# Performance work log

Measured on AMD Instinct MI355X. Metric: run time of the kernel, lower is better.

## Reference

```python
import jax, jax.numpy as jnp
import numpy as np

N_NODES = 100000


def setup_inputs() -> dict:
    key = jax.random.key(0)
    ks = jax.random.split(key, 8)
    E = 1600000
    x = jax.random.normal(ks[0], (N_NODES, 128), dtype=jnp.float32)
    src = jax.random.randint(ks[1], (E,), 0, N_NODES, dtype=jnp.int32)
    dst = jax.random.randint(ks[2], (E,), 0, N_NODES, dtype=jnp.int32)
    s = 1.0 / np.sqrt(128.0)
    w_self = jax.random.normal(ks[3], (5, 128, 128), dtype=jnp.float32) * s
    w_neigh = jax.random.normal(ks[4], (5, 128, 128), dtype=jnp.float32) * s
    b = jnp.zeros((5, 128), dtype=jnp.float32)
    w_self_out = jax.random.normal(ks[5], (128, 47), dtype=jnp.float32) * s
    w_neigh_out = jax.random.normal(ks[6], (128, 47), dtype=jnp.float32) * s
    b_out = jnp.zeros((47,), dtype=jnp.float32)
    return {"x": x, "src": src, "dst": dst, "w_self": w_self, "w_neigh": w_neigh,
            "b": b, "w_self_out": w_self_out, "w_neigh_out": w_neigh_out, "b_out": b_out}


def _mean_agg(h, src, dst, inv_deg):
    # segment-sum of source features into destination nodes, then mean
    summed = jax.ops.segment_sum(h[src], dst, num_segments=N_NODES)  # [N, d]
    return summed * inv_deg[:, None]


def _sage_layer(h, src, dst, inv_deg, ws, wn, bias):
    neigh = _mean_agg(h, src, dst, inv_deg)
    return h @ ws + neigh @ wn + bias


def reference(x, src, dst, w_self, w_neigh, b, w_self_out, w_neigh_out, b_out):
    # in-degree, clamped to 1 for isolated nodes (DGL mean aggregator behavior)
    deg = jax.ops.segment_sum(jnp.ones_like(dst, dtype=x.dtype), dst, num_segments=N_NODES)
    inv_deg = 1.0 / jnp.maximum(deg, 1.0)

    # layer 0: no ReLU after (matches original forward)
    h = _sage_layer(x, src, dst, inv_deg, w_self[0], w_neigh[0], b[0])
    # layers 1..4: SAGEConv + ReLU
    for i in range(1, 5):
        h = _sage_layer(h, src, dst, inv_deg, w_self[i], w_neigh[i], b[i])
        h = jax.nn.relu(h)
    # final layer: 128 -> num_classes, no activation
    h = _sage_layer(h, src, dst, inv_deg, w_self_out, w_neigh_out, b_out)
    return h
```

## Files before the change

kernel.cpp:

```cpp
#include <hip/hip_runtime.h>

typedef float f4 __attribute__((ext_vector_type(4)));
typedef float f32x4 __attribute__((ext_vector_type(4)));
typedef float f2 __attribute__((ext_vector_type(2)));
typedef short s16x8 __attribute__((ext_vector_type(8)));
typedef int i4 __attribute__((ext_vector_type(4)));

#define N_NODES 100000
#define NBUCK 196
#define NB1 256

__device__ inline unsigned short f2bf(float f) {
    unsigned int u = __builtin_bit_cast(unsigned int, f);
    u += 0x7FFFu + ((u >> 16) & 1u);
    return (unsigned short)(u >> 16);
}
__device__ inline float bflo(unsigned int v) { return __builtin_bit_cast(float, v << 16); }
__device__ inline float bfhi(unsigned int v) { return __builtin_bit_cast(float, v & 0xFFFF0000u); }


__global__ __launch_bounds__(256) void k_hist(const int* __restrict__ dst,
                                              int* __restrict__ histG, int E) {
    __shared__ int h[NBUCK];
    int tid = threadIdx.x;
    for (int i = tid; i < NBUCK; i += 256) h[i] = 0;
    __syncthreads();
    int chunk = (E + NB1 - 1) / NB1;
    int s = blockIdx.x * chunk, eN = min(E, s + chunk);
    for (int i = s + tid; i < eN; i += 256) atomicAdd(&h[dst[i] >> 9], 1);
    __syncthreads();
    for (int i = tid; i < NBUCK; i += 256) histG[i * NB1 + blockIdx.x] = h[i];
}

__global__ __launch_bounds__(1024) void k_scanB(int* __restrict__ histG) {
    __shared__ int ps[1024];
    int t = threadIdx.x;
    int base = t * 49;
    int vals[49];
    int sum = 0;
#pragma unroll
    for (int i = 0; i < 49; ++i) { vals[i] = histG[base + i]; sum += vals[i]; }
    ps[t] = sum;
    __syncthreads();
    for (int off = 1; off < 1024; off <<= 1) {
        int v = (t >= off) ? ps[t - off] : 0;
        __syncthreads();
        ps[t] += v;
        __syncthreads();
    }
    int run = ps[t] - sum;
#pragma unroll
    for (int i = 0; i < 49; ++i) { int v = vals[i]; histG[base + i] = run; run += v; }
}

__global__ __launch_bounds__(256) void k_place(const int* __restrict__ src,
                                               const int* __restrict__ dst,
                                               const int* __restrict__ histG,
                                               unsigned int* __restrict__ ebuf, int E) {
    __shared__ int cur[NBUCK];
    int tid = threadIdx.x;
    for (int i = tid; i < NBUCK; i += 256) cur[i] = histG[i * NB1 + blockIdx.x];
    __syncthreads();
    int chunk = (E + NB1 - 1) / NB1;
    int s = blockIdx.x * chunk, eN = min(E, s + chunk);
    for (int i = s + tid; i < eN; i += 256) {
        int d = dst[i];
        int b = d >> 9;
        int pos = atomicAdd(&cur[b], 1);
        ebuf[pos] = (unsigned int)src[i] | ((unsigned int)(d & 511) << 17);
    }
}

__global__ __launch_bounds__(256) void k_csr(const unsigned int* __restrict__ ebuf,
                                             const int* __restrict__ histG,
                                             int* __restrict__ rp, int* __restrict__ col,
                                             float* __restrict__ invd, int N, int E) {
    __shared__ int ldeg[512];
    __shared__ int lbase[512];
    int b = blockIdx.x, tid = threadIdx.x;
    int base = histG[b * NB1];
    int endB = (b == NBUCK - 1) ? E : histG[(b + 1) * NB1];
    int cnt = endB - base;
    int n0 = b << 9;

    ldeg[tid] = 0;
    ldeg[tid + 256] = 0;
    __syncthreads();
    for (int i = tid; i < cnt; i += 256) atomicAdd(&ldeg[ebuf[base + i] >> 17], 1);
    __syncthreads();

    int a0 = ldeg[tid], a1 = ldeg[tid + 256];
    lbase[tid] = a0;
    lbase[tid + 256] = a1;
    __syncthreads();
    for (int off = 1; off < 512; off <<= 1) {
        int v0 = (tid >= off) ? lbase[tid - off] : 0;
        int v1 = (tid + 256 >= off) ? lbase[tid + 256 - off] : 0;
        __syncthreads();
        lbase[tid] += v0;
        lbase[tid + 256] += v1;
        __syncthreads();
    }
    int e0 = lbase[tid] - a0, e1 = lbase[tid + 256] - a1;
    __syncthreads();
    lbase[tid] = e0;
    lbase[tid + 256] = e1;
    ldeg[tid] = 0;
    ldeg[tid + 256] = 0;
    __syncthreads();

    for (int i = tid; i < cnt; i += 256) {
        unsigned int p = ebuf[base + i];
        int dl = p >> 17;
        int pos = base + lbase[dl] + atomicAdd(&ldeg[dl], 1);
        col[pos] = (int)(p & 0x1FFFFu) << 8;
    }

    int g0 = n0 + tid, g1 = n0 + tid + 256;
    if (g0 < N) { rp[g0] = base + e0; invd[g0] = 1.0f / fmaxf((float)a0, 1.0f); }
    if (g1 < N) { rp[g1] = base + e1; invd[g1] = 1.0f / fmaxf((float)a1, 1.0f); }
    if (b == NBUCK - 1 && tid == 0) rp[N] = E;
}


__global__ void k_cvt(const float* __restrict__ x, unsigned short* __restrict__ xb, int n8) {
    int t = blockIdx.x * 256 + threadIdx.x;
    if (t >= n8) return;
    f4 a = *(const f4*)&x[(size_t)t * 8];
    f4 b = *(const f4*)&x[(size_t)t * 8 + 4];
    s16x8 p;
    p[0] = (short)f2bf(a[0]); p[1] = (short)f2bf(a[1]);
    p[2] = (short)f2bf(a[2]); p[3] = (short)f2bf(a[3]);
    p[4] = (short)f2bf(b[0]); p[5] = (short)f2bf(b[1]);
    p[6] = (short)f2bf(b[2]); p[7] = (short)f2bf(b[3]);
    *(s16x8*)&xb[(size_t)t * 8] = p;
}

__global__ void k_prepw(const float* __restrict__ ws, const float* __restrict__ wn,
                        unsigned short* __restrict__ wp) {
    int t = blockIdx.x * 256 + threadIdx.x;
    if (t >= 5 * 4096) return;
    int l = t & 63, nfg = (t >> 6) & 7, ks = (t >> 9) & 7, lyr = t >> 12;
    int n = nfg * 16 + (l & 15);
    s16x8 p;
#pragma unroll
    for (int j = 0; j < 8; ++j) {
        int k = ks * 32 + (l >> 4) * 8 + j;
        float v = (k < 128) ? ws[((size_t)lyr * 128 + k) * 128 + n]
                            : wn[((size_t)lyr * 128 + (k - 128)) * 128 + n];
        p[j] = (short)f2bf(v);
    }
    *(s16x8*)&wp[(size_t)t * 8] = p;
}

__global__ void k_prepwo(const float* __restrict__ wso, const float* __restrict__ wno,
                         unsigned short* __restrict__ wpo) {
    int t = blockIdx.x * 256 + threadIdx.x;
    if (t >= 1536) return;
    int l = t & 63, q = t >> 6;
    int nf = q % 3, ks = q / 3;
    int n = nf * 16 + (l & 15);
    s16x8 p;
#pragma unroll
    for (int j = 0; j < 8; ++j) {
        int k = ks * 32 + (l >> 4) * 8 + j;
        float v = 0.f;
        if (n < 47) v = (k < 128) ? wso[(size_t)k * 47 + n] : wno[(size_t)(k - 128) * 47 + n];
        p[j] = (short)f2bf(v);
    }
    *(s16x8*)&wpo[(size_t)t * 8] = p;
}


__global__ __launch_bounds__(256) void k_agg(const unsigned short* __restrict__ h,
                                             const int* __restrict__ rp,
                                             const int* __restrict__ col,
                                             const float* __restrict__ invd,
                                             unsigned short* __restrict__ out, int n) {
    int gw = (blockIdx.x * 256 + threadIdx.x) >> 6;
    int lane = threadIdx.x & 63;
    if (gw >= n) return;
    const char* hb = (const char*)h;
    const int lb = lane * 4;
    int beg = rp[gw], end = rp[gw + 1];
    f2 acc = {0.f, 0.f};
    int e = beg;
    for (; e + 8 <= end; e += 8) {
        i4 c0, c1;
        __builtin_memcpy(&c0, &col[e], 16);
        __builtin_memcpy(&c1, &col[e + 4], 16);
        unsigned int u[8];
#pragma unroll
        for (int i = 0; i < 4; ++i)
            u[i] = *(const unsigned int*)(hb + (unsigned int)(c0[i] + lb));
#pragma unroll
        for (int i = 0; i < 4; ++i)
            u[4 + i] = *(const unsigned int*)(hb + (unsigned int)(c1[i] + lb));
#pragma unroll
        for (int i = 0; i < 8; ++i) {
            f2 v = {bflo(u[i]), bfhi(u[i])};
            acc += v;
        }
    }
    if (e < end) {
        int rem = end - e;
        i4 c0, c1;
        __builtin_memcpy(&c0, &col[e], 16);
        __builtin_memcpy(&c1, &col[e + 4], 16);
        unsigned int u[8];
#pragma unroll
        for (int i = 0; i < 4; ++i)
            u[i] = *(const unsigned int*)(hb + (unsigned int)(c0[i] + lb));
#pragma unroll
        for (int i = 0; i < 4; ++i)
            u[4 + i] = *(const unsigned int*)(hb + (unsigned int)(c1[i] + lb));
#pragma unroll
        for (int i = 0; i < 8; ++i) {
            if (i < rem) {
                f2 v = {bflo(u[i]), bfhi(u[i])};
                acc += v;
            }
        }
    }
    float iv = invd[gw];
    unsigned int r = (unsigned int)f2bf(acc[0] * iv) | ((unsigned int)f2bf(acc[1] * iv) << 16);
    ((unsigned int*)out)[(size_t)gw * 64 + lane] = r;
}


__global__ __launch_bounds__(256) void gemm128(const unsigned short* __restrict__ h,
                                               const unsigned short* __restrict__ nb,
                                               const unsigned short* __restrict__ wl,
                                               const float* __restrict__ bias,
                                               unsigned short* __restrict__ out,
                                               int M, int relu) {
    __shared__ s16x8 afr[4096];
    const int tid = threadIdx.x;
    const int l = tid & 63, w = tid >> 6;
    const int r0 = blockIdx.x * 128;
    const int cg = (w * 4 + (l >> 4)) * 8;

    s16x8 th[8], tn[8];
#pragma unroll
    for (int i = 0; i < 8; ++i) {
        int r = r0 + i * 16 + (l & 15);
        if (r >= M) r = M - 1;
        th[i] = *(const s16x8*)(h + (size_t)r * 128 + cg);
        tn[i] = *(const s16x8*)(nb + (size_t)r * 128 + cg);
    }
#pragma unroll
    for (int i = 0; i < 8; ++i) {
        afr[(w * 8 + i) * 64 + l] = th[i];
        afr[((w + 4) * 8 + i) * 64 + l] = tn[i];
    }
    __syncthreads();

    const int mh = w >> 1, nh = w & 1;
    const s16x8* wf = (const s16x8*)wl;

    f32x4 acc[4][4];
#pragma unroll
    for (int i = 0; i < 4; ++i)
#pragma unroll
        for (int j = 0; j < 4; ++j) acc[i][j] = (f32x4)0.f;

#pragma unroll
    for (int ks = 0; ks < 8; ++ks) {
        s16x8 bw[4], ha[4];
#pragma unroll
        for (int nf = 0; nf < 4; ++nf) bw[nf] = wf[(ks * 8 + nh * 4 + nf) * 64 + l];
#pragma unroll
        for (int mf = 0; mf < 4; ++mf) ha[mf] = afr[(ks * 8 + mh * 4 + mf) * 64 + l];
#pragma unroll
        for (int mf = 0; mf < 4; ++mf)
#pragma unroll
            for (int nf = 0; nf < 4; ++nf)
                acc[mf][nf] = __builtin_amdgcn_mfma_f32_16x16x32_bf16(bw[nf], ha[mf],
                                                                      acc[mf][nf], 0, 0, 0);
    }

    f4 bv[4];
#pragma unroll
    for (int nf = 0; nf < 4; ++nf)
        bv[nf] = *(const f4*)&bias[nh * 64 + nf * 16 + ((l >> 4) << 2)];

#pragma unroll
    for (int mf = 0; mf < 4; ++mf) {
        int row = r0 + mh * 64 + mf * 16 + (l & 15);
        if (row >= M) continue;
#pragma unroll
        for (int nf = 0; nf < 4; ++nf) {
            int ncol = nh * 64 + nf * 16 + ((l >> 4) << 2);
            f32x4 a = acc[mf][nf];
            float v0 = a[0] + bv[nf][0], v1 = a[1] + bv[nf][1];
            float v2 = a[2] + bv[nf][2], v3 = a[3] + bv[nf][3];
            if (relu) {
                v0 = fmaxf(v0, 0.f); v1 = fmaxf(v1, 0.f);
                v2 = fmaxf(v2, 0.f); v3 = fmaxf(v3, 0.f);
            }
            uint2 p;
            p.x = (unsigned int)f2bf(v0) | ((unsigned int)f2bf(v1) << 16);
            p.y = (unsigned int)f2bf(v2) | ((unsigned int)f2bf(v3) << 16);
            *(uint2*)(out + (size_t)row * 128 + ncol) = p;
        }
    }
}


__global__ __launch_bounds__(256) void gemm_out47(const unsigned short* __restrict__ h,
                                                  const unsigned short* __restrict__ nb,
                                                  const unsigned short* __restrict__ wpo,
                                                  const float* __restrict__ bo,
                                                  float* __restrict__ out, int M) {
    __shared__ s16x8 afr[4096];
    const int tid = threadIdx.x;
    const int l = tid & 63, w = tid >> 6;
    const int r0 = blockIdx.x * 128;
    const int cg = (w * 4 + (l >> 4)) * 8;

    s16x8 th[8], tn[8];
#pragma unroll
    for (int i = 0; i < 8; ++i) {
        int r = r0 + i * 16 + (l & 15);
        if (r >= M) r = M - 1;
        th[i] = *(const s16x8*)(h + (size_t)r * 128 + cg);
        tn[i] = *(const s16x8*)(nb + (size_t)r * 128 + cg);
    }
#pragma unroll
    for (int i = 0; i < 8; ++i) {
        afr[(w * 8 + i) * 64 + l] = th[i];
        afr[((w + 4) * 8 + i) * 64 + l] = tn[i];
    }
    __syncthreads();

    const s16x8* wf = (const s16x8*)wpo;
    f32x4 acc[2][3];
#pragma unroll
    for (int i = 0; i < 2; ++i)
#pragma unroll
        for (int j = 0; j < 3; ++j) acc[i][j] = (f32x4)0.f;

#pragma unroll
    for (int ks = 0; ks < 8; ++ks) {
        s16x8 bw[3], ha[2];
#pragma unroll
        for (int nf = 0; nf < 3; ++nf) bw[nf] = wf[(ks * 3 + nf) * 64 + l];
#pragma unroll
        for (int mf = 0; mf < 2; ++mf) ha[mf] = afr[(ks * 8 + w * 2 + mf) * 64 + l];
#pragma unroll
        for (int mf = 0; mf < 2; ++mf)
#pragma unroll
            for (int nf = 0; nf < 3; ++nf)
                acc[mf][nf] = __builtin_amdgcn_mfma_f32_16x16x32_bf16(bw[nf], ha[mf],
                                                                      acc[mf][nf], 0, 0, 0);
    }

#pragma unroll
    for (int mf = 0; mf < 2; ++mf) {
        int row = r0 + w * 32 + mf * 16 + (l & 15);
        if (row >= M) continue;
#pragma unroll
        for (int nf = 0; nf < 3; ++nf) {
            int ncol = nf * 16 + ((l >> 4) << 2);
            f32x4 a = acc[mf][nf];
#pragma unroll
            for (int jj = 0; jj < 4; ++jj) {
                int n = ncol + jj;
                if (n < 47) out[(size_t)row * 47 + n] = a[jj] + bo[n];
            }
        }
    }
}


static inline char* alignp(char* p) {
    return (char*)(((size_t)p + 255) & ~(size_t)255);
}

extern "C" void kernel_launch(void* const* d_in, const int* in_sizes, int n_in,
                              void* d_out, int out_size, void* d_ws, size_t ws_size,
                              hipStream_t stream) {
    const float* x = (const float*)d_in[0];
    const int* src = (const int*)d_in[1];
    const int* dst = (const int*)d_in[2];
    const float* w_self = (const float*)d_in[3];
    const float* w_neigh = (const float*)d_in[4];
    const float* b = (const float*)d_in[5];
    const float* wso = (const float*)d_in[6];
    const float* wno = (const float*)d_in[7];
    const float* bo = (const float*)d_in[8];
    float* out = (float*)d_out;

    const int N = N_NODES;
    const int E = in_sizes[1];

    char* w = (char*)d_ws;
    unsigned short* xb = (unsigned short*)w;  w = alignp(w + (size_t)N * 128 * 2);
    unsigned short* hA = (unsigned short*)w;  w = alignp(w + (size_t)N * 128 * 2);
    unsigned short* hB = (unsigned short*)w;  w = alignp(w + (size_t)N * 128 * 2);
    unsigned short* wp = (unsigned short*)w;  w = alignp(w + (size_t)5 * 32768 * 2);
    unsigned short* wpo = (unsigned short*)w; w = alignp(w + (size_t)1536 * 8 * 2);
    int* rp = (int*)w;       w = alignp(w + (size_t)(N + 4) * 4);
    int* col = (int*)w;      w = alignp(w + (size_t)E * 4);
    int* histG = (int*)w;    w = alignp(w + (size_t)NBUCK * NB1 * 4);
    float* invd = (float*)w; w = alignp(w + (size_t)N * 4);

    unsigned int* ebuf = (unsigned int*)hB;

    k_hist<<<NB1, 256, 0, stream>>>(dst, histG, E);
    k_scanB<<<1, 1024, 0, stream>>>(histG);
    k_place<<<NB1, 256, 0, stream>>>(src, dst, histG, ebuf, E);
    k_csr<<<NBUCK, 256, 0, stream>>>(ebuf, histG, rp, col, invd, N, E);

    k_cvt<<<(N * 128 / 8 + 255) / 256, 256, 0, stream>>>(x, xb, N * 128 / 8);
    k_prepw<<<(5 * 4096 + 255) / 256, 256, 0, stream>>>(w_self, w_neigh, wp);
    k_prepwo<<<6, 256, 0, stream>>>(wso, wno, wpo);

    const int aggBlocks = (N * 64 + 255) / 256;
    const int gemmBlocks = (N + 127) / 128;

    k_agg<<<aggBlocks, 256, 0, stream>>>(xb, rp, col, invd, hA, N);
    gemm128<<<gemmBlocks, 256, 0, stream>>>(xb, hA, wp, b, hA, N, 0);

    unsigned short* cur = hA;
    unsigned short* oth = hB;
    for (int lyr = 1; lyr < 5; ++lyr) {
        k_agg<<<aggBlocks, 256, 0, stream>>>(cur, rp, col, invd, oth, N);
        gemm128<<<gemmBlocks, 256, 0, stream>>>(cur, oth, wp + (size_t)lyr * 32768,
                                                b + (size_t)lyr * 128, oth, N, 1);
        unsigned short* t = cur; cur = oth; oth = t;
    }

    k_agg<<<aggBlocks, 256, 0, stream>>>(cur, rp, col, invd, oth, N);
    gemm_out47<<<gemmBlocks, 256, 0, stream>>>(cur, oth, wpo, bo, out, N);
}
```

Baseline: 578.8 us.

## Project before aggregating in final layer and stream GEMM A-fragments directly

```diff
diff --git a/kernel.cpp b/kernel.cpp
--- a/kernel.cpp
+++ b/kernel.cpp
@@ -120,6 +120,7 @@
     if (g0 < N) { rp[g0] = base + e0; invd[g0] = 1.0f / fmaxf((float)a0, 1.0f); }
     if (g1 < N) { rp[g1] = base + e1; invd[g1] = 1.0f / fmaxf((float)a1, 1.0f); }
     if (b == NBUCK - 1 && tid == 0) rp[N] = E;
+    if (b == NBUCK - 1 && tid < 32) col[E + tid] = 0;
 }
 
 
@@ -154,21 +155,24 @@
 }
 
 __global__ void k_prepwo(const float* __restrict__ wso, const float* __restrict__ wno,
-                         unsigned short* __restrict__ wpo) {
+                         unsigned short* __restrict__ wS, unsigned short* __restrict__ wN,
+                         const float* __restrict__ bo, float* __restrict__ bo48) {
     int t = blockIdx.x * 256 + threadIdx.x;
-    if (t >= 1536) return;
-    int l = t & 63, q = t >> 6;
-    int nf = q % 3, ks = q / 3;
+    if (t < 48) bo48[t] = (t < 47) ? bo[t] : 0.f;
+    if (t >= 2 * 768) return;
+    int tbl = t / 768, r = t % 768;
+    int ks = r / 192, nf = (r / 64) % 3, l = r & 63;
     int n = nf * 16 + (l & 15);
+    const float* W = tbl ? wno : wso;
+    unsigned short* dstp = tbl ? wN : wS;
     s16x8 p;
 #pragma unroll
     for (int j = 0; j < 8; ++j) {
         int k = ks * 32 + (l >> 4) * 8 + j;
-        float v = 0.f;
-        if (n < 47) v = (k < 128) ? wso[(size_t)k * 47 + n] : wno[(size_t)(k - 128) * 47 + n];
+        float v = (n < 47) ? W[(size_t)k * 47 + n] : 0.f;
         p[j] = (short)f2bf(v);
     }
-    *(s16x8*)&wpo[(size_t)t * 8] = p;
+    *(s16x8*)&dstp[(size_t)r * 8] = p;
 }
 
 
@@ -228,55 +232,46 @@
 }
 
 
-__global__ __launch_bounds__(256) void gemm128(const unsigned short* __restrict__ h,
-                                               const unsigned short* __restrict__ nb,
-                                               const unsigned short* __restrict__ wl,
-                                               const float* __restrict__ bias,
-                                               unsigned short* __restrict__ out,
-                                               int M, int relu) {
-    __shared__ s16x8 afr[4096];
+__global__ __launch_bounds__(256) void gemm128d(const unsigned short* __restrict__ h,
+                                                const unsigned short* __restrict__ nb,
+                                                const unsigned short* __restrict__ wl,
+                                                const float* __restrict__ bias,
+                                                unsigned short* __restrict__ out,
+                                                int M, int relu) {
     const int tid = threadIdx.x;
-    const int l = tid & 63, w = tid >> 6;
-    const int r0 = blockIdx.x * 128;
-    const int cg = (w * 4 + (l >> 4)) * 8;
-
-    s16x8 th[8], tn[8];
-#pragma unroll
-    for (int i = 0; i < 8; ++i) {
-        int r = r0 + i * 16 + (l & 15);
-        if (r >= M) r = M - 1;
-        th[i] = *(const s16x8*)(h + (size_t)r * 128 + cg);
-        tn[i] = *(const s16x8*)(nb + (size_t)r * 128 + cg);
-    }
-#pragma unroll
-    for (int i = 0; i < 8; ++i) {
-        afr[(w * 8 + i) * 64 + l] = th[i];
-        afr[((w + 4) * 8 + i) * 64 + l] = tn[i];
-    }
-    __syncthreads();
-
-    const int mh = w >> 1, nh = w & 1;
+    const int l = tid & 63, wv = tid >> 6;
+    const int mh = wv >> 1, nh = wv & 1;
+    const int r0 = blockIdx.x * 64;
     const s16x8* wf = (const s16x8*)wl;
-
-    f32x4 acc[4][4];
-#pragma unroll
-    for (int i = 0; i < 4; ++i)
+    const int cgb = (l >> 4) << 3;
+
+    int R[2];
+#pragma unroll
+    for (int mf = 0; mf < 2; ++mf) {
+        int r = r0 + mh * 32 + mf * 16 + (l & 15);
+        R[mf] = (r > M - 1) ? (M - 1) : r;
+    }
+
+    f32x4 acc[2][4];
+#pragma unroll
+    for (int i = 0; i < 2; ++i)
 #pragma unroll
         for (int j = 0; j < 4; ++j) acc[i][j] = (f32x4)0.f;
 
 #pragma unroll
     for (int ks = 0; ks < 8; ++ks) {
-        s16x8 bw[4], ha[4];
-#pragma unroll
-        for (int nf = 0; nf < 4; ++nf) bw[nf] = wf[(ks * 8 + nh * 4 + nf) * 64 + l];
-#pragma unroll
-        for (int mf = 0; mf < 4; ++mf) ha[mf] = afr[(ks * 8 + mh * 4 + mf) * 64 + l];
-#pragma unroll
-        for (int mf = 0; mf < 4; ++mf)
-#pragma unroll
-            for (int nf = 0; nf < 4; ++nf)
-                acc[mf][nf] = __builtin_amdgcn_mfma_f32_16x16x32_bf16(bw[nf], ha[mf],
-                                                                      acc[mf][nf], 0, 0, 0);
+        const unsigned short* A = (ks < 4) ? h : nb;
+        const int kk = ks & 3;
+        s16x8 ha[2];
+#pragma unroll
+        for (int mf = 0; mf < 2; ++mf)
+            ha[mf] = *(const s16x8*)(A + (size_t)R[mf] * 128 + kk * 32 + cgb);
+#pragma unroll
+        for (int nf = 0; nf < 4; ++nf) {
+            s16x8 bw = wf[(ks * 8 + nh * 4 + nf) * 64 + l];
+            acc[0][nf] = __builtin_amdgcn_mfma_f32_16x16x32_bf16(bw, ha[0], acc[0][nf], 0, 0, 0);
+            acc[1][nf] = __builtin_amdgcn_mfma_f32_16x16x32_bf16(bw, ha[1], acc[1][nf], 0, 0, 0);
+        }
     }
 
     f4 bv[4];
@@ -285,8 +280,8 @@
         bv[nf] = *(const f4*)&bias[nh * 64 + nf * 16 + ((l >> 4) << 2)];
 
 #pragma unroll
-    for (int mf = 0; mf < 4; ++mf) {
-        int row = r0 + mh * 64 + mf * 16 + (l & 15);
+    for (int mf = 0; mf < 2; ++mf) {
+        int row = r0 + mh * 32 + mf * 16 + (l & 15);
         if (row >= M) continue;
 #pragma unroll
         for (int nf = 0; nf < 4; ++nf) {
@@ -307,33 +302,26 @@
 }
 
 
-__global__ __launch_bounds__(256) void gemm_out47(const unsigned short* __restrict__ h,
-                                                  const unsigned short* __restrict__ nb,
-                                                  const unsigned short* __restrict__ wpo,
-                                                  const float* __restrict__ bo,
-                                                  float* __restrict__ out, int M) {
-    __shared__ s16x8 afr[4096];
+__global__ __launch_bounds__(256) void gemm_fin(const unsigned short* __restrict__ h,
+                                                const unsigned short* __restrict__ wS,
+                                                const unsigned short* __restrict__ wN,
+                                                const float* __restrict__ bo48,
+                                                unsigned short* __restrict__ tmpn,
+                                                float* __restrict__ selfo, int M) {
     const int tid = threadIdx.x;
-    const int l = tid & 63, w = tid >> 6;
-    const int r0 = blockIdx.x * 128;
-    const int cg = (w * 4 + (l >> 4)) * 8;
-
-    s16x8 th[8], tn[8];
-#pragma unroll
-    for (int i = 0; i < 8; ++i) {
-        int r = r0 + i * 16 + (l & 15);
-        if (r >= M) r = M - 1;
-        th[i] = *(const s16x8*)(h + (size_t)r * 128 + cg);
-        tn[i] = *(const s16x8*)(nb + (size_t)r * 128 + cg);
-    }
-#pragma unroll
-    for (int i = 0; i < 8; ++i) {
-        afr[(w * 8 + i) * 64 + l] = th[i];
-        afr[((w + 4) * 8 + i) * 64 + l] = tn[i];
-    }
-    __syncthreads();
-
-    const s16x8* wf = (const s16x8*)wpo;
+    const int l = tid & 63, wv = tid >> 6;
+    const int mh = wv >> 1, sel = wv & 1;
+    const int r0 = blockIdx.x * 64;
+    const s16x8* wf = (const s16x8*)(sel ? wN : wS);
+    const int cgb = (l >> 4) << 3;
+
+    int R[2];
+#pragma unroll
+    for (int mf = 0; mf < 2; ++mf) {
+        int r = r0 + mh * 32 + mf * 16 + (l & 15);
+        R[mf] = (r > M - 1) ? (M - 1) : r;
+    }
+
     f32x4 acc[2][3];
 #pragma unroll
     for (int i = 0; i < 2; ++i)
@@ -341,34 +329,91 @@
         for (int j = 0; j < 3; ++j) acc[i][j] = (f32x4)0.f;
 
 #pragma unroll
-    for (int ks = 0; ks < 8; ++ks) {
-        s16x8 bw[3], ha[2];
-#pragma unroll
-        for (int nf = 0; nf < 3; ++nf) bw[nf] = wf[(ks * 3 + nf) * 64 + l];
-#pragma unroll
-        for (int mf = 0; mf < 2; ++mf) ha[mf] = afr[(ks * 8 + w * 2 + mf) * 64 + l];
+    for (int ks = 0; ks < 4; ++ks) {
+        s16x8 ha[2];
 #pragma unroll
         for (int mf = 0; mf < 2; ++mf)
-#pragma unroll
-            for (int nf = 0; nf < 3; ++nf)
-                acc[mf][nf] = __builtin_amdgcn_mfma_f32_16x16x32_bf16(bw[nf], ha[mf],
-                                                                      acc[mf][nf], 0, 0, 0);
+            ha[mf] = *(const s16x8*)(h + (size_t)R[mf] * 128 + ks * 32 + cgb);
+#pragma unroll
+        for (int nf = 0; nf < 3; ++nf) {
+            s16x8 bw = wf[(ks * 3 + nf) * 64 + l];
+            acc[0][nf] = __builtin_amdgcn_mfma_f32_16x16x32_bf16(bw, ha[0], acc[0][nf], 0, 0, 0);
+            acc[1][nf] = __builtin_amdgcn_mfma_f32_16x16x32_bf16(bw, ha[1], acc[1][nf], 0, 0, 0);
+        }
     }
 
 #pragma unroll
     for (int mf = 0; mf < 2; ++mf) {
-        int row = r0 + w * 32 + mf * 16 + (l & 15);
+        int row = r0 + mh * 32 + mf * 16 + (l & 15);
         if (row >= M) continue;
 #pragma unroll
         for (int nf = 0; nf < 3; ++nf) {
             int ncol = nf * 16 + ((l >> 4) << 2);
             f32x4 a = acc[mf][nf];
-#pragma unroll
-            for (int jj = 0; jj < 4; ++jj) {
-                int n = ncol + jj;
-                if (n < 47) out[(size_t)row * 47 + n] = a[jj] + bo[n];
+            if (sel == 0) {
+                f4 bv = *(const f4*)&bo48[ncol];
+                f4 o;
+                o[0] = a[0] + bv[0]; o[1] = a[1] + bv[1];
+                o[2] = a[2] + bv[2]; o[3] = a[3] + bv[3];
+                *(f4*)&selfo[(size_t)row * 48 + ncol] = o;
+            } else {
+                uint2 p;
+                p.x = (unsigned int)f2bf(a[0]) | ((unsigned int)f2bf(a[1]) << 16);
+                p.y = (unsigned int)f2bf(a[2]) | ((unsigned int)f2bf(a[3]) << 16);
+                *(uint2*)(tmpn + (size_t)row * 64 + ncol) = p;
             }
         }
+    }
+}
+
+
+__global__ __launch_bounds__(256) void k_agg_fin(const unsigned short* __restrict__ z,
+                                                 const float* __restrict__ selfo,
+                                                 const int* __restrict__ rp,
+                                                 const int* __restrict__ col,
+                                                 const float* __restrict__ invd,
+                                                 float* __restrict__ out, int n) {
+    int gw = (blockIdx.x * 256 + threadIdx.x) >> 6;
+    int lane = threadIdx.x & 63;
+    if (gw >= n) return;
+    const char* zb = (const char*)z;
+    const int hhalf = lane >> 5;
+    const int lb = (lane & 31) * 4;
+    int beg = rp[gw], end = rp[gw + 1];
+    f2 acc = {0.f, 0.f};
+    int e = beg;
+    for (; e + 8 <= end; e += 8) {
+        unsigned int u[4];
+#pragma unroll
+        for (int j = 0; j < 4; ++j) {
+            unsigned int c = (unsigned int)col[e + 2 * j + hhalf];
+            u[j] = *(const unsigned int*)(zb + (c >> 1) + lb);
+        }
+#pragma unroll
+        for (int j = 0; j < 4; ++j) { f2 v = {bflo(u[j]), bfhi(u[j])}; acc += v; }
+    }
+    if (e < end) {
+        int rem = end - e;
+        unsigned int u[4];
+#pragma unroll
+        for (int j = 0; j < 4; ++j) {
+            unsigned int c = (unsigned int)col[e + 2 * j + hhalf];
+            u[j] = *(const unsigned int*)(zb + (c >> 1) + lb);
+        }
+#pragma unroll
+        for (int j = 0; j < 4; ++j) {
+            if (2 * j + hhalf < rem) { f2 v = {bflo(u[j]), bfhi(u[j])}; acc += v; }
+        }
+    }
+    f2 tot;
+    tot[0] = acc[0] + __shfl_xor(acc[0], 32);
+    tot[1] = acc[1] + __shfl_xor(acc[1], 32);
+    float iv = invd[gw];
+    if (lane < 24) {
+        int c0 = lane * 2;
+        f2 s = *(const f2*)&selfo[(size_t)gw * 48 + c0];
+        out[(size_t)gw * 47 + c0] = s[0] + tot[0] * iv;
+        if (c0 + 1 < 47) out[(size_t)gw * 47 + c0 + 1] = s[1] + tot[1] * iv;
     }
 }
 
@@ -395,17 +440,21 @@
     const int E = in_sizes[1];
 
     char* w = (char*)d_ws;
-    unsigned short* xb = (unsigned short*)w;  w = alignp(w + (size_t)N * 128 * 2);
-    unsigned short* hA = (unsigned short*)w;  w = alignp(w + (size_t)N * 128 * 2);
-    unsigned short* hB = (unsigned short*)w;  w = alignp(w + (size_t)N * 128 * 2);
-    unsigned short* wp = (unsigned short*)w;  w = alignp(w + (size_t)5 * 32768 * 2);
-    unsigned short* wpo = (unsigned short*)w; w = alignp(w + (size_t)1536 * 8 * 2);
+    unsigned short* xb = (unsigned short*)w;   w = alignp(w + (size_t)N * 128 * 2);
+    unsigned short* hA = (unsigned short*)w;   w = alignp(w + (size_t)N * 128 * 2);
+    unsigned short* hB = (unsigned short*)w;   w = alignp(w + (size_t)N * 128 * 2);
+    unsigned short* nbuf = (unsigned short*)w; w = alignp(w + (size_t)N * 128 * 2);
+    unsigned short* wp = (unsigned short*)w;   w = alignp(w + (size_t)5 * 32768 * 2);
+    unsigned short* wS = (unsigned short*)w;   w = alignp(w + (size_t)768 * 8 * 2);
+    unsigned short* wN = (unsigned short*)w;   w = alignp(w + (size_t)768 * 8 * 2);
+    float* bo48 = (float*)w; w = alignp(w + 48 * 4);
     int* rp = (int*)w;       w = alignp(w + (size_t)(N + 4) * 4);
-    int* col = (int*)w;      w = alignp(w + (size_t)E * 4);
+    int* col = (int*)w;      w = alignp(w + (size_t)(E + 32) * 4);
     int* histG = (int*)w;    w = alignp(w + (size_t)NBUCK * NB1 * 4);
     float* invd = (float*)w; w = alignp(w + (size_t)N * 4);
 
     unsigned int* ebuf = (unsigned int*)hB;
+    unsigned short* tmpn = nbuf;
 
     k_hist<<<NB1, 256, 0, stream>>>(dst, histG, E);
     k_scanB<<<1, 1024, 0, stream>>>(histG);
@@ -414,23 +463,24 @@
 
     k_cvt<<<(N * 128 / 8 + 255) / 256, 256, 0, stream>>>(x, xb, N * 128 / 8);
     k_prepw<<<(5 * 4096 + 255) / 256, 256, 0, stream>>>(w_self, w_neigh, wp);
-    k_prepwo<<<6, 256, 0, stream>>>(wso, wno, wpo);
+    k_prepwo<<<6, 256, 0, stream>>>(wso, wno, wS, wN, bo, bo48);
 
     const int aggBlocks = (N * 64 + 255) / 256;
-    const int gemmBlocks = (N + 127) / 128;
-
-    k_agg<<<aggBlocks, 256, 0, stream>>>(xb, rp, col, invd, hA, N);
-    gemm128<<<gemmBlocks, 256, 0, stream>>>(xb, hA, wp, b, hA, N, 0);
+    const int gemmBlocks = (N + 63) / 64;
+
+    k_agg<<<aggBlocks, 256, 0, stream>>>(xb, rp, col, invd, nbuf, N);
+    gemm128d<<<gemmBlocks, 256, 0, stream>>>(xb, nbuf, wp, b, hA, N, 0);
 
     unsigned short* cur = hA;
     unsigned short* oth = hB;
     for (int lyr = 1; lyr < 5; ++lyr) {
-        k_agg<<<aggBlocks, 256, 0, stream>>>(cur, rp, col, invd, oth, N);
-        gemm128<<<gemmBlocks, 256, 0, stream>>>(cur, oth, wp + (size_t)lyr * 32768,
-                                                b + (size_t)lyr * 128, oth, N, 1);
+        k_agg<<<aggBlocks, 256, 0, stream>>>(cur, rp, col, invd, nbuf, N);
+        gemm128d<<<gemmBlocks, 256, 0, stream>>>(cur, nbuf, wp + (size_t)lyr * 32768,
+                                                 b + (size_t)lyr * 128, oth, N, 1);
         unsigned short* t = cur; cur = oth; oth = t;
     }
 
-    k_agg<<<aggBlocks, 256, 0, stream>>>(cur, rp, col, invd, oth, N);
-    gemm_out47<<<gemmBlocks, 256, 0, stream>>>(cur, oth, wpo, bo, out, N);
-}
+    float* selfo = (float*)hB;
+    gemm_fin<<<gemmBlocks, 256, 0, stream>>>(cur, wS, wN, bo48, tmpn, selfo, N);
+    k_agg_fin<<<aggBlocks, 256, 0, stream>>>(tmpn, selfo, rp, col, invd, out, N);
+}
```

After: 578.9 us. Within noise of the previous version (+0.0%).
